# Kernel optimization log

Measured on AMD Instinct MI355X. Metric: run time of the kernel, lower is better.

Reference implementation:

```python
import jax, jax.numpy as jnp
import numpy as np

# Each of the 16 soft binary logic ops is a polynomial c0 + c1*a + c2*b + c3*a*b.
# Rows below are the [c0, c1, c2, c3] coefficients for ops 0..15 (same math as bin_op).
_OP_COEF = np.array([
    [0., 0., 0., 0.],   # 0: zeros
    [0., 0., 0., 1.],   # 1: a*b
    [0., 1., 0., -1.],  # 2: a - a*b
    [0., 1., 0., 0.],   # 3: a
    [0., 0., 1., -1.],  # 4: b - a*b
    [0., 0., 1., 0.],   # 5: b
    [0., 1., 1., -2.],  # 6: a + b - 2ab
    [0., 1., 1., -1.],  # 7: a + b - ab
    [1., -1., -1., 1.], # 8: 1 - (a + b - ab)
    [1., -1., -1., 2.], # 9: 1 - (a + b - 2ab)
    [1., 0., -1., 0.],  # 10: 1 - b
    [1., 0., -1., 1.],  # 11: 1 - b + ab
    [1., -1., 0., 0.],  # 12: 1 - a
    [1., -1., 0., 1.],  # 13: 1 - a + ab
    [1., 0., 0., -1.],  # 14: 1 - a*b
    [1., 0., 0., 0.],   # 15: ones
], dtype=np.float32)

K_CLASSES = 10
TAU = 30.0


def logic_layer(x, w, idx_a, idx_b):
    # x: [B, in_dim], w: [out_dim, 16], idx_a/idx_b: [out_dim]
    probs = jax.nn.softmax(w, axis=-1)                 # [O, 16]
    coef = probs @ jnp.asarray(_OP_COEF)               # [O, 4]
    a = x[:, idx_a]                                    # [B, O]
    b = x[:, idx_b]                                    # [B, O]
    # weighted mixture of 16 ops == polynomial in (1, a, b, a*b)
    return coef[:, 0] + coef[:, 1] * a + coef[:, 2] * b + coef[:, 3] * (a * b)


def group_sum(x, k, tau):
    B = x.shape[0]
    return x.reshape(B, k, x.shape[-1] // k).sum(-1) / tau


def setup_inputs() -> dict:
    key = jax.random.key(0)
    ks = jax.random.split(key, 10)
    B, D0, D1, D2, D3 = 4096, 1024, 8192, 8192, 10240
    return {
        "x": jax.random.uniform(ks[0], (B, D0), dtype=jnp.float32),
        "w1": jax.random.normal(ks[1], (D1, 16), dtype=jnp.float32),
        "w2": jax.random.normal(ks[2], (D2, 16), dtype=jnp.float32),
        "w3": jax.random.normal(ks[3], (D3, 16), dtype=jnp.float32),
        "idx_a1": jax.random.randint(ks[4], (D1,), 0, D0, dtype=jnp.int32),
        "idx_b1": jax.random.randint(ks[5], (D1,), 0, D0, dtype=jnp.int32),
        "idx_a2": jax.random.randint(ks[6], (D2,), 0, D1, dtype=jnp.int32),
        "idx_b2": jax.random.randint(ks[7], (D2,), 0, D1, dtype=jnp.int32),
        "idx_a3": jax.random.randint(ks[8], (D3,), 0, D2, dtype=jnp.int32),
        "idx_b3": jax.random.randint(ks[9], (D3,), 0, D2, dtype=jnp.int32),
    }


def reference(x, w1, w2, w3, idx_a1, idx_b1, idx_a2, idx_b2, idx_a3, idx_b3):
    h = logic_layer(x, w1, idx_a1, idx_b1)
    h = logic_layer(h, w2, idx_a2, idx_b2)
    h = logic_layer(h, w3, idx_a3, idx_b3)
    return group_sum(h, K_CLASSES, TAU)   # [B, 10]
```

## Files before the change

kernel.cpp:

```cpp
#include <hip/hip_runtime.h>
#include <hip/hip_fp16.h>
#include <stdint.h>

#define D0 1024
#define D1 8192
#define D2 8192
#define D3 10240
#define B_ROWS 4096

#define SM_XB     0
#define SM_H2     8192
#define SM_CSUM   (8192 + 65536)
#define SM_BYTES  (8192 + 65536 + 160)

__device__ __forceinline__ float4 softmax_coef(const float* __restrict__ w) {
    const float4* wv = (const float4*)w;
    float4 q0 = wv[0], q1 = wv[1], q2 = wv[2], q3 = wv[3];
    float wa[16] = {q0.x, q0.y, q0.z, q0.w, q1.x, q1.y, q1.z, q1.w,
                    q2.x, q2.y, q2.z, q2.w, q3.x, q3.y, q3.z, q3.w};
    float m = wa[0];
#pragma unroll
    for (int i = 1; i < 16; ++i) m = fmaxf(m, wa[i]);
    float e[16], s = 0.f;
#pragma unroll
    for (int i = 0; i < 16; ++i) { e[i] = __expf(wa[i] - m); s += e[i]; }
    float inv = 1.f / s;
    static constexpr float OPC[16][4] = {
        {0.f, 0.f, 0.f, 0.f}, {0.f, 0.f, 0.f, 1.f}, {0.f, 1.f, 0.f, -1.f}, {0.f, 1.f, 0.f, 0.f},
        {0.f, 0.f, 1.f, -1.f}, {0.f, 0.f, 1.f, 0.f}, {0.f, 1.f, 1.f, -2.f}, {0.f, 1.f, 1.f, -1.f},
        {1.f, -1.f, -1.f, 1.f}, {1.f, -1.f, -1.f, 2.f}, {1.f, 0.f, -1.f, 0.f}, {1.f, 0.f, -1.f, 1.f},
        {1.f, -1.f, 0.f, 0.f}, {1.f, -1.f, 0.f, 1.f}, {1.f, 0.f, 0.f, -1.f}, {1.f, 0.f, 0.f, 0.f}};
    float c0 = 0.f, c1 = 0.f, c2 = 0.f, c3 = 0.f;
#pragma unroll
    for (int i = 0; i < 16; ++i) {
        float p = e[i] * inv;
        c0 += p * OPC[i][0];
        c1 += p * OPC[i][1];
        c2 += p * OPC[i][2];
        c3 += p * OPC[i][3];
    }
    return make_float4(c0, c1, c2, c3);
}

__device__ __forceinline__ uint2 pack_coef(float4 c) {
    uint2 r;
    r.x = __builtin_bit_cast(uint32_t, __floats2half2_rn(c.x, c.y));
    r.y = __builtin_bit_cast(uint32_t, __floats2half2_rn(c.z, c.w));
    return r;
}

__global__ __launch_bounds__(64) void prep_kernel(
    const float* __restrict__ w1, const float* __restrict__ w2,
    const float* __restrict__ w3,
    const int* __restrict__ ia1, const int* __restrict__ ib1,
    const int* __restrict__ ia2, const int* __restrict__ ib2,
    const int* __restrict__ ia3, const int* __restrict__ ib3,
    uint2* __restrict__ bcIdx, uint4* __restrict__ bcCoefAB,
    uint2* __restrict__ bcCoefO, uint32_t* __restrict__ d3Idx,
    uint2* __restrict__ d3Coef) {
    int G = blockIdx.x * 64 + threadIdx.x;
    if (G < D2) {
        int g = G;
        int pa = ia2[g], pb = ib2[g];
        float4 cO = softmax_coef(w2 + (size_t)g * 16);
        float4 cA = softmax_coef(w1 + (size_t)pa * 16);
        float4 cB = softmax_coef(w1 + (size_t)pb * 16);
        uint2 xi;
        xi.x = (uint32_t)(ia1[pa] << 3) | ((uint32_t)(ib1[pa] << 3) << 16);
        xi.y = (uint32_t)(ia1[pb] << 3) | ((uint32_t)(ib1[pb] << 3) << 16);
        bcIdx[g] = xi;
        uint2 a = pack_coef(cA), b = pack_coef(cB);
        bcCoefAB[g] = make_uint4(a.x, a.y, b.x, b.y);
        bcCoefO[g] = pack_coef(cO);
    } else {
        int g = G - D2;
        float4 cO = softmax_coef(w3 + (size_t)g * 16);
        d3Idx[g] = (uint32_t)(ia3[g] << 3) | ((uint32_t)(ib3[g] << 3) << 16);
        d3Coef[g] = pack_coef(cO);
    }
}

__device__ __forceinline__ uint2 gate4(uint2 av, uint2 bv, uint2 cf) {
    __half2 p = __builtin_bit_cast(__half2, cf.x);
    __half2 q = __builtin_bit_cast(__half2, cf.y);
    __half2 c0 = __low2half2(p), c1 = __high2half2(p);
    __half2 c2 = __low2half2(q), c3 = __high2half2(q);
    __half2 a01 = __builtin_bit_cast(__half2, av.x);
    __half2 a23 = __builtin_bit_cast(__half2, av.y);
    __half2 b01 = __builtin_bit_cast(__half2, bv.x);
    __half2 b23 = __builtin_bit_cast(__half2, bv.y);
    __half2 h01 = __hfma2(a01, __hfma2(b01, c3, c1), __hfma2(b01, c2, c0));
    __half2 h23 = __hfma2(a23, __hfma2(b23, c3, c1), __hfma2(b23, c2, c0));
    uint2 r;
    r.x = __builtin_bit_cast(uint32_t, h01);
    r.y = __builtin_bit_cast(uint32_t, h23);
    return r;
}

__global__ __launch_bounds__(1024, 8) void fused_kernel(
    const float* __restrict__ x, const uint2* __restrict__ bcIdx,
    const uint4* __restrict__ bcCoefAB, const uint2* __restrict__ bcCoefO,
    const uint32_t* __restrict__ d3Idx, const uint2* __restrict__ d3Coef,
    float* __restrict__ out) {
    extern __shared__ char sm[];
    uint2* xb = (uint2*)(sm + SM_XB);
    uint2* h2 = (uint2*)(sm + SM_H2);
    float* csum = (float*)(sm + SM_CSUM);

    const int t = threadIdx.x;
    const int rowbase = blockIdx.x << 2;

    {
        const float* xp = x + (size_t)rowbase * D0 + t;
        float v0 = xp[0];
        float v1 = xp[D0];
        float v2 = xp[2 * D0];
        float v3 = xp[3 * D0];
        uint2 v;
        v.x = __builtin_bit_cast(uint32_t, __floats2half2_rn(v0, v1));
        v.y = __builtin_bit_cast(uint32_t, __floats2half2_rn(v2, v3));
        xb[t] = v;
    }
    if (t < 40) csum[t] = 0.f;
    __syncthreads();

    for (int k = 0; k < 8; ++k) {
        int g = t + (k << 10);
        uint2 xi = bcIdx[g];
        uint4 cab = bcCoefAB[g];
        uint2 co = bcCoefO[g];
        uint2 aa = *(const uint2*)(sm + (xi.x & 0xffffu));
        uint2 ab = *(const uint2*)(sm + (xi.x >> 16));
        uint2 ba = *(const uint2*)(sm + (xi.y & 0xffffu));
        uint2 bb = *(const uint2*)(sm + (xi.y >> 16));
        uint2 ha = gate4(aa, ab, make_uint2(cab.x, cab.y));
        uint2 hb = gate4(ba, bb, make_uint2(cab.z, cab.w));
        h2[g] = gate4(ha, hb, co);
    }
    __syncthreads();

    {
        const int wv = t >> 6, lane = t & 63;
        const int gbase = wv * 640;
        const int cA = gbase >> 10;
        const int bnd = (cA + 1) << 10;
        float s0[4] = {0.f, 0.f, 0.f, 0.f};
        float s1[4] = {0.f, 0.f, 0.f, 0.f};
#pragma unroll
        for (int j = 0; j < 10; ++j) {
            int gc = gbase + (j << 6);
            int g = gc + lane;
            uint32_t ip = d3Idx[g];
            uint2 cf = d3Coef[g];
            uint2 av = *(const uint2*)(sm + SM_H2 + (ip & 0xffffu));
            uint2 bv = *(const uint2*)(sm + SM_H2 + (ip >> 16));
            uint2 hv = gate4(av, bv, cf);
            __half2 h01 = __builtin_bit_cast(__half2, hv.x);
            __half2 h23 = __builtin_bit_cast(__half2, hv.y);
            float f0 = __low2float(h01), f1 = __high2float(h01);
            float f2 = __low2float(h23), f3 = __high2float(h23);
            if (gc < bnd) {
                s0[0] += f0; s0[1] += f1; s0[2] += f2; s0[3] += f3;
            } else {
                s1[0] += f0; s1[1] += f1; s1[2] += f2; s1[3] += f3;
            }
        }
#pragma unroll
        for (int m = 1; m < 64; m <<= 1) {
#pragma unroll
            for (int r = 0; r < 4; ++r) {
                s0[r] += __shfl_xor(s0[r], m, 64);
                s1[r] += __shfl_xor(s1[r], m, 64);
            }
        }
        if (lane == 0) {
#pragma unroll
            for (int r = 0; r < 4; ++r) atomicAdd(&csum[cA * 4 + r], s0[r]);
            if (gbase + 640 > bnd) {
#pragma unroll
                for (int r = 0; r < 4; ++r) atomicAdd(&csum[(cA + 1) * 4 + r], s1[r]);
            }
        }
    }
    __syncthreads();

    if (t < 40) {
        int c = t >> 2, r = t & 3;
        out[(size_t)(rowbase + r) * 10 + c] = csum[t] * (1.0f / 30.0f);
    }
}

extern "C" void kernel_launch(void* const* d_in, const int* in_sizes, int n_in,
                              void* d_out, int out_size, void* d_ws, size_t ws_size,
                              hipStream_t stream) {
    const float* x = (const float*)d_in[0];
    const float* w1 = (const float*)d_in[1];
    const float* w2 = (const float*)d_in[2];
    const float* w3 = (const float*)d_in[3];
    const int* ia1 = (const int*)d_in[4];
    const int* ib1 = (const int*)d_in[5];
    const int* ia2 = (const int*)d_in[6];
    const int* ib2 = (const int*)d_in[7];
    const int* ia3 = (const int*)d_in[8];
    const int* ib3 = (const int*)d_in[9];
    float* out = (float*)d_out;

    char* p = (char*)d_ws;
    uint2* bcIdx = (uint2*)p;                 p += (size_t)D2 * 8;
    uint4* bcCoefAB = (uint4*)p;              p += (size_t)D2 * 16;
    uint2* bcCoefO = (uint2*)p;               p += (size_t)D2 * 8;
    uint32_t* d3Idx = (uint32_t*)p;           p += (size_t)D3 * 4;
    uint2* d3Coef = (uint2*)p;

    hipFuncSetAttribute(reinterpret_cast<const void*>(fused_kernel),
                        hipFuncAttributeMaxDynamicSharedMemorySize, SM_BYTES);

    prep_kernel<<<(D2 + D3) / 64, 64, 0, stream>>>(
        w1, w2, w3, ia1, ib1, ia2, ib2, ia3, ib3,
        bcIdx, bcCoefAB, bcCoefO, d3Idx, d3Coef);
    fused_kernel<<<B_ROWS / 4, 1024, SM_BYTES, stream>>>(
        x, bcIdx, bcCoefAB, bcCoefO, d3Idx, d3Coef, out);
}
```

Baseline: 107.1 us.

## Pack per-gate metadata into uint4 records and process two gates per thread

Per-gate indices and fp16 coefficients are repacked into 16-byte records. Layer-1/2 uses two arrays (index plus output coef, and A/B coefs), and layer 3 uses one padded record array. Each thread now handles two adjacent gates per iteration with 128-bit loads and prefetches the next iteration's index record before the x staging. This cuts global load instruction count and exposes more memory-level parallelism. In exchange the layer-3 data grows through padding, register pressure rises, and pairs of outputs are summed in fp16 before the float accumulation.

```diff
diff --git a/kernel.cpp b/kernel.cpp
--- a/kernel.cpp
+++ b/kernel.cpp
@@ -55,9 +55,8 @@
     const int* __restrict__ ia1, const int* __restrict__ ib1,
     const int* __restrict__ ia2, const int* __restrict__ ib2,
     const int* __restrict__ ia3, const int* __restrict__ ib3,
-    uint2* __restrict__ bcIdx, uint4* __restrict__ bcCoefAB,
-    uint2* __restrict__ bcCoefO, uint32_t* __restrict__ d3Idx,
-    uint2* __restrict__ d3Coef) {
+    uint4* __restrict__ bcM1, uint4* __restrict__ bcM2,
+    uint4* __restrict__ d3M) {
     int G = blockIdx.x * 64 + threadIdx.x;
     if (G < D2) {
         int g = G;
@@ -65,18 +64,17 @@
         float4 cO = softmax_coef(w2 + (size_t)g * 16);
         float4 cA = softmax_coef(w1 + (size_t)pa * 16);
         float4 cB = softmax_coef(w1 + (size_t)pb * 16);
-        uint2 xi;
-        xi.x = (uint32_t)(ia1[pa] << 3) | ((uint32_t)(ib1[pa] << 3) << 16);
-        xi.y = (uint32_t)(ia1[pb] << 3) | ((uint32_t)(ib1[pb] << 3) << 16);
-        bcIdx[g] = xi;
-        uint2 a = pack_coef(cA), b = pack_coef(cB);
-        bcCoefAB[g] = make_uint4(a.x, a.y, b.x, b.y);
-        bcCoefO[g] = pack_coef(cO);
+        uint32_t xiA = (uint32_t)(ia1[pa] << 3) | ((uint32_t)(ib1[pa] << 3) << 16);
+        uint32_t xiB = (uint32_t)(ia1[pb] << 3) | ((uint32_t)(ib1[pb] << 3) << 16);
+        uint2 o = pack_coef(cO), a = pack_coef(cA), b = pack_coef(cB);
+        bcM1[g] = make_uint4(xiA, xiB, o.x, o.y);
+        bcM2[g] = make_uint4(a.x, a.y, b.x, b.y);
     } else {
         int g = G - D2;
         float4 cO = softmax_coef(w3 + (size_t)g * 16);
-        d3Idx[g] = (uint32_t)(ia3[g] << 3) | ((uint32_t)(ib3[g] << 3) << 16);
-        d3Coef[g] = pack_coef(cO);
+        uint2 o = pack_coef(cO);
+        uint32_t xi = (uint32_t)(ia3[g] << 3) | ((uint32_t)(ib3[g] << 3) << 16);
+        d3M[g] = make_uint4(xi, o.x, o.y, 0u);
     }
 }
 
@@ -98,17 +96,19 @@
 }
 
 __global__ __launch_bounds__(1024, 8) void fused_kernel(
-    const float* __restrict__ x, const uint2* __restrict__ bcIdx,
-    const uint4* __restrict__ bcCoefAB, const uint2* __restrict__ bcCoefO,
-    const uint32_t* __restrict__ d3Idx, const uint2* __restrict__ d3Coef,
+    const float* __restrict__ x, const uint4* __restrict__ bcM1,
+    const uint4* __restrict__ bcM2, const uint4* __restrict__ d3M,
     float* __restrict__ out) {
     extern __shared__ char sm[];
     uint2* xb = (uint2*)(sm + SM_XB);
-    uint2* h2 = (uint2*)(sm + SM_H2);
     float* csum = (float*)(sm + SM_CSUM);
 
     const int t = threadIdx.x;
     const int rowbase = blockIdx.x << 2;
+    const int tg = t << 1;
+
+    uint4 m1a_n = bcM1[tg];
+    uint4 m1b_n = bcM1[tg + 1];
 
     {
         const float* xp = x + (size_t)rowbase * D0 + t;
@@ -124,18 +124,32 @@
     if (t < 40) csum[t] = 0.f;
     __syncthreads();
 
-    for (int k = 0; k < 8; ++k) {
-        int g = t + (k << 10);
-        uint2 xi = bcIdx[g];
-        uint4 cab = bcCoefAB[g];
-        uint2 co = bcCoefO[g];
-        uint2 aa = *(const uint2*)(sm + (xi.x & 0xffffu));
-        uint2 ab = *(const uint2*)(sm + (xi.x >> 16));
-        uint2 ba = *(const uint2*)(sm + (xi.y & 0xffffu));
-        uint2 bb = *(const uint2*)(sm + (xi.y >> 16));
-        uint2 ha = gate4(aa, ab, make_uint2(cab.x, cab.y));
-        uint2 hb = gate4(ba, bb, make_uint2(cab.z, cab.w));
-        h2[g] = gate4(ha, hb, co);
+#pragma unroll
+    for (int k = 0; k < 4; ++k) {
+        uint4 m1a = m1a_n, m1b = m1b_n;
+        int g = tg + (k << 11);
+        uint4 m2a = bcM2[g];
+        uint4 m2b = bcM2[g + 1];
+        if (k < 3) {
+            int gn = tg + ((k + 1) << 11);
+            m1a_n = bcM1[gn];
+            m1b_n = bcM1[gn + 1];
+        }
+        uint2 aa0 = *(const uint2*)(sm + (m1a.x & 0xffffu));
+        uint2 ab0 = *(const uint2*)(sm + (m1a.x >> 16));
+        uint2 ba0 = *(const uint2*)(sm + (m1a.y & 0xffffu));
+        uint2 bb0 = *(const uint2*)(sm + (m1a.y >> 16));
+        uint2 aa1 = *(const uint2*)(sm + (m1b.x & 0xffffu));
+        uint2 ab1 = *(const uint2*)(sm + (m1b.x >> 16));
+        uint2 ba1 = *(const uint2*)(sm + (m1b.y & 0xffffu));
+        uint2 bb1 = *(const uint2*)(sm + (m1b.y >> 16));
+        uint2 h0 = gate4(gate4(aa0, ab0, make_uint2(m2a.x, m2a.y)),
+                         gate4(ba0, bb0, make_uint2(m2a.z, m2a.w)),
+                         make_uint2(m1a.z, m1a.w));
+        uint2 h1v = gate4(gate4(aa1, ab1, make_uint2(m2b.x, m2b.y)),
+                          gate4(ba1, bb1, make_uint2(m2b.z, m2b.w)),
+                          make_uint2(m1b.z, m1b.w));
+        ((uint4*)(sm + SM_H2))[(k << 10) + t] = make_uint4(h0.x, h0.y, h1v.x, h1v.y);
     }
     __syncthreads();
 
@@ -147,18 +161,23 @@
         float s0[4] = {0.f, 0.f, 0.f, 0.f};
         float s1[4] = {0.f, 0.f, 0.f, 0.f};
 #pragma unroll
-        for (int j = 0; j < 10; ++j) {
-            int gc = gbase + (j << 6);
-            int g = gc + lane;
-            uint32_t ip = d3Idx[g];
-            uint2 cf = d3Coef[g];
-            uint2 av = *(const uint2*)(sm + SM_H2 + (ip & 0xffffu));
-            uint2 bv = *(const uint2*)(sm + SM_H2 + (ip >> 16));
-            uint2 hv = gate4(av, bv, cf);
-            __half2 h01 = __builtin_bit_cast(__half2, hv.x);
-            __half2 h23 = __builtin_bit_cast(__half2, hv.y);
-            float f0 = __low2float(h01), f1 = __high2float(h01);
-            float f2 = __low2float(h23), f3 = __high2float(h23);
+        for (int j = 0; j < 5; ++j) {
+            int gc = gbase + (j << 7);
+            int g = gc + (lane << 1);
+            uint4 ma = d3M[g];
+            uint4 mb = d3M[g + 1];
+            uint2 av0 = *(const uint2*)(sm + SM_H2 + (ma.x & 0xffffu));
+            uint2 bv0 = *(const uint2*)(sm + SM_H2 + (ma.x >> 16));
+            uint2 av1 = *(const uint2*)(sm + SM_H2 + (mb.x & 0xffffu));
+            uint2 bv1 = *(const uint2*)(sm + SM_H2 + (mb.x >> 16));
+            uint2 h0 = gate4(av0, bv0, make_uint2(ma.y, ma.z));
+            uint2 h1v = gate4(av1, bv1, make_uint2(mb.y, mb.z));
+            __half2 p01 = __hadd2(__builtin_bit_cast(__half2, h0.x),
+                                  __builtin_bit_cast(__half2, h1v.x));
+            __half2 p23 = __hadd2(__builtin_bit_cast(__half2, h0.y),
+                                  __builtin_bit_cast(__half2, h1v.y));
+            float f0 = __low2float(p01), f1 = __high2float(p01);
+            float f2 = __low2float(p23), f3 = __high2float(p23);
             if (gc < bnd) {
                 s0[0] += f0; s0[1] += f1; s0[2] += f2; s0[3] += f3;
             } else {
@@ -206,18 +225,14 @@
     float* out = (float*)d_out;
 
     char* p = (char*)d_ws;
-    uint2* bcIdx = (uint2*)p;                 p += (size_t)D2 * 8;
-    uint4* bcCoefAB = (uint4*)p;              p += (size_t)D2 * 16;
-    uint2* bcCoefO = (uint2*)p;               p += (size_t)D2 * 8;
-    uint32_t* d3Idx = (uint32_t*)p;           p += (size_t)D3 * 4;
-    uint2* d3Coef = (uint2*)p;
+    uint4* bcM1 = (uint4*)p;    p += (size_t)D2 * 16;
+    uint4* bcM2 = (uint4*)p;    p += (size_t)D2 * 16;
+    uint4* d3M = (uint4*)p;
 
     hipFuncSetAttribute(reinterpret_cast<const void*>(fused_kernel),
                         hipFuncAttributeMaxDynamicSharedMemorySize, SM_BYTES);
 
     prep_kernel<<<(D2 + D3) / 64, 64, 0, stream>>>(
-        w1, w2, w3, ia1, ib1, ia2, ib2, ia3, ib3,
-        bcIdx, bcCoefAB, bcCoefO, d3Idx, d3Coef);
-    fused_kernel<<<B_ROWS / 4, 1024, SM_BYTES, stream>>>(
-        x, bcIdx, bcCoefAB, bcCoefO, d3Idx, d3Coef, out);
-}
+        w1, w2, w3, ia1, ib1, ia2, ib2, ia3, ib3, bcM1, bcM2, d3M);
+    fused_kernel<<<B_ROWS / 4, 1024, SM_BYTES, stream>>>(x, bcM1, bcM2, d3M, out);
+}
```

Result: no change. 106.9 us (-0.2%).

## Recompute layer-2 gates per layer-3 output to eliminate shared intermediate buffer

Applied to the files above, without the earlier changes.

Flattens the three-layer gate tree so each layer-3 output directly gathers its four layer-1 input pairs from the staged input row, recomputing layer-1 and layer-2 gates instead of storing layer-2 results in shared memory. The prep kernel now precomputes per-output composite index and coefficient tables, and the main kernel uses 512 threads with about 8 KB of LDS and one fewer barrier. This trades roughly double gate arithmetic and more metadata loads for much higher occupancy and less LDS traffic.

```diff
diff --git a/kernel.cpp b/kernel.cpp
--- a/kernel.cpp
+++ b/kernel.cpp
@@ -7,11 +7,6 @@
 #define D2 8192
 #define D3 10240
 #define B_ROWS 4096
-
-#define SM_XB     0
-#define SM_H2     8192
-#define SM_CSUM   (8192 + 65536)
-#define SM_BYTES  (8192 + 65536 + 160)
 
 __device__ __forceinline__ float4 softmax_coef(const float* __restrict__ w) {
     const float4* wv = (const float4*)w;
@@ -49,35 +44,33 @@
     return r;
 }
 
-__global__ __launch_bounds__(64) void prep_kernel(
+__global__ __launch_bounds__(256) void prep_kernel(
     const float* __restrict__ w1, const float* __restrict__ w2,
     const float* __restrict__ w3,
     const int* __restrict__ ia1, const int* __restrict__ ib1,
     const int* __restrict__ ia2, const int* __restrict__ ib2,
     const int* __restrict__ ia3, const int* __restrict__ ib3,
-    uint2* __restrict__ bcIdx, uint4* __restrict__ bcCoefAB,
-    uint2* __restrict__ bcCoefO, uint32_t* __restrict__ d3Idx,
-    uint2* __restrict__ d3Coef) {
-    int G = blockIdx.x * 64 + threadIdx.x;
-    if (G < D2) {
-        int g = G;
-        int pa = ia2[g], pb = ib2[g];
-        float4 cO = softmax_coef(w2 + (size_t)g * 16);
-        float4 cA = softmax_coef(w1 + (size_t)pa * 16);
-        float4 cB = softmax_coef(w1 + (size_t)pb * 16);
-        uint2 xi;
-        xi.x = (uint32_t)(ia1[pa] << 3) | ((uint32_t)(ib1[pa] << 3) << 16);
-        xi.y = (uint32_t)(ia1[pb] << 3) | ((uint32_t)(ib1[pb] << 3) << 16);
-        bcIdx[g] = xi;
-        uint2 a = pack_coef(cA), b = pack_coef(cB);
-        bcCoefAB[g] = make_uint4(a.x, a.y, b.x, b.y);
-        bcCoefO[g] = pack_coef(cO);
-    } else {
-        int g = G - D2;
-        float4 cO = softmax_coef(w3 + (size_t)g * 16);
-        d3Idx[g] = (uint32_t)(ia3[g] << 3) | ((uint32_t)(ib3[g] << 3) << 16);
-        d3Coef[g] = pack_coef(cO);
-    }
+    uint4* __restrict__ M0, uint4* __restrict__ M1, uint4* __restrict__ M2,
+    uint4* __restrict__ M3, uint2* __restrict__ M4) {
+    int g = blockIdx.x * 256 + threadIdx.x;
+    int p0 = ia3[g], p1 = ib3[g];
+    int a0 = ia2[p0], b0 = ib2[p0];
+    int a1 = ia2[p1], b1 = ib2[p1];
+    uint32_t x0 = (uint32_t)(ia1[a0] << 3) | ((uint32_t)(ib1[a0] << 3) << 16);
+    uint32_t x1 = (uint32_t)(ia1[b0] << 3) | ((uint32_t)(ib1[b0] << 3) << 16);
+    uint32_t x2 = (uint32_t)(ia1[a1] << 3) | ((uint32_t)(ib1[a1] << 3) << 16);
+    uint32_t x3 = (uint32_t)(ia1[b1] << 3) | ((uint32_t)(ib1[b1] << 3) << 16);
+    M0[g] = make_uint4(x0, x1, x2, x3);
+    uint2 cA0 = pack_coef(softmax_coef(w1 + (size_t)a0 * 16));
+    uint2 cB0 = pack_coef(softmax_coef(w1 + (size_t)b0 * 16));
+    M1[g] = make_uint4(cA0.x, cA0.y, cB0.x, cB0.y);
+    uint2 cA1 = pack_coef(softmax_coef(w1 + (size_t)a1 * 16));
+    uint2 cB1 = pack_coef(softmax_coef(w1 + (size_t)b1 * 16));
+    M2[g] = make_uint4(cA1.x, cA1.y, cB1.x, cB1.y);
+    uint2 cP0 = pack_coef(softmax_coef(w2 + (size_t)p0 * 16));
+    uint2 cP1 = pack_coef(softmax_coef(w2 + (size_t)p1 * 16));
+    M3[g] = make_uint4(cP0.x, cP0.y, cP1.x, cP1.y);
+    M4[g] = pack_coef(softmax_coef(w3 + (size_t)g * 16));
 }
 
 __device__ __forceinline__ uint2 gate4(uint2 av, uint2 bv, uint2 cf) {
@@ -97,89 +90,87 @@
     return r;
 }
 
-__global__ __launch_bounds__(1024, 8) void fused_kernel(
-    const float* __restrict__ x, const uint2* __restrict__ bcIdx,
-    const uint4* __restrict__ bcCoefAB, const uint2* __restrict__ bcCoefO,
-    const uint32_t* __restrict__ d3Idx, const uint2* __restrict__ d3Coef,
+__global__ __launch_bounds__(512, 8) void fused_kernel(
+    const float* __restrict__ x, const uint4* __restrict__ M0,
+    const uint4* __restrict__ M1, const uint4* __restrict__ M2,
+    const uint4* __restrict__ M3, const uint2* __restrict__ M4,
     float* __restrict__ out) {
-    extern __shared__ char sm[];
-    uint2* xb = (uint2*)(sm + SM_XB);
-    uint2* h2 = (uint2*)(sm + SM_H2);
-    float* csum = (float*)(sm + SM_CSUM);
+    __shared__ char sm[8192 + 160];
+    uint2* xb = (uint2*)sm;
+    float* csum = (float*)(sm + 8192);
 
     const int t = threadIdx.x;
     const int rowbase = blockIdx.x << 2;
+    const int wv = t >> 6, lane = t & 63;
+    const int gbase = wv * 1280;
+
+    uint4 m0_n = M0[gbase + lane];
 
     {
-        const float* xp = x + (size_t)rowbase * D0 + t;
-        float v0 = xp[0];
-        float v1 = xp[D0];
-        float v2 = xp[2 * D0];
-        float v3 = xp[3 * D0];
-        uint2 v;
-        v.x = __builtin_bit_cast(uint32_t, __floats2half2_rn(v0, v1));
-        v.y = __builtin_bit_cast(uint32_t, __floats2half2_rn(v2, v3));
-        xb[t] = v;
+        const float* xp = x + (size_t)rowbase * D0;
+#pragma unroll
+        for (int c = t; c < D0; c += 512) {
+            uint2 v;
+            v.x = __builtin_bit_cast(uint32_t, __floats2half2_rn(xp[c], xp[D0 + c]));
+            v.y = __builtin_bit_cast(uint32_t, __floats2half2_rn(xp[2 * D0 + c], xp[3 * D0 + c]));
+            xb[c] = v;
+        }
     }
     if (t < 40) csum[t] = 0.f;
     __syncthreads();
 
-    for (int k = 0; k < 8; ++k) {
-        int g = t + (k << 10);
-        uint2 xi = bcIdx[g];
-        uint4 cab = bcCoefAB[g];
-        uint2 co = bcCoefO[g];
-        uint2 aa = *(const uint2*)(sm + (xi.x & 0xffffu));
-        uint2 ab = *(const uint2*)(sm + (xi.x >> 16));
-        uint2 ba = *(const uint2*)(sm + (xi.y & 0xffffu));
-        uint2 bb = *(const uint2*)(sm + (xi.y >> 16));
-        uint2 ha = gate4(aa, ab, make_uint2(cab.x, cab.y));
-        uint2 hb = gate4(ba, bb, make_uint2(cab.z, cab.w));
-        h2[g] = gate4(ha, hb, co);
-    }
-    __syncthreads();
-
-    {
-        const int wv = t >> 6, lane = t & 63;
-        const int gbase = wv * 640;
-        const int cA = gbase >> 10;
-        const int bnd = (cA + 1) << 10;
-        float s0[4] = {0.f, 0.f, 0.f, 0.f};
-        float s1[4] = {0.f, 0.f, 0.f, 0.f};
-#pragma unroll
-        for (int j = 0; j < 10; ++j) {
-            int gc = gbase + (j << 6);
-            int g = gc + lane;
-            uint32_t ip = d3Idx[g];
-            uint2 cf = d3Coef[g];
-            uint2 av = *(const uint2*)(sm + SM_H2 + (ip & 0xffffu));
-            uint2 bv = *(const uint2*)(sm + SM_H2 + (ip >> 16));
-            uint2 hv = gate4(av, bv, cf);
-            __half2 h01 = __builtin_bit_cast(__half2, hv.x);
-            __half2 h23 = __builtin_bit_cast(__half2, hv.y);
-            float f0 = __low2float(h01), f1 = __high2float(h01);
-            float f2 = __low2float(h23), f3 = __high2float(h23);
-            if (gc < bnd) {
-                s0[0] += f0; s0[1] += f1; s0[2] += f2; s0[3] += f3;
-            } else {
-                s1[0] += f0; s1[1] += f1; s1[2] += f2; s1[3] += f3;
-            }
-        }
-#pragma unroll
-        for (int m = 1; m < 64; m <<= 1) {
-#pragma unroll
-            for (int r = 0; r < 4; ++r) {
-                s0[r] += __shfl_xor(s0[r], m, 64);
-                s1[r] += __shfl_xor(s1[r], m, 64);
-            }
-        }
-        if (lane == 0) {
-#pragma unroll
-            for (int r = 0; r < 4; ++r) atomicAdd(&csum[cA * 4 + r], s0[r]);
-            if (gbase + 640 > bnd) {
-#pragma unroll
-                for (int r = 0; r < 4; ++r) atomicAdd(&csum[(cA + 1) * 4 + r], s1[r]);
-            }
+    const int cA = gbase >> 10;
+    const int bnd = (cA + 1) << 10;
+    float s0[4] = {0.f, 0.f, 0.f, 0.f};
+    float s1[4] = {0.f, 0.f, 0.f, 0.f};
+#pragma unroll
+    for (int j = 0; j < 20; ++j) {
+        int g = gbase + (j << 6) + lane;
+        uint4 m0 = m0_n;
+        if (j < 19) m0_n = M0[g + 64];
+        uint2 aa = *(const uint2*)(sm + (m0.x & 0xffffu));
+        uint2 ab = *(const uint2*)(sm + (m0.x >> 16));
+        uint2 ba = *(const uint2*)(sm + (m0.y & 0xffffu));
+        uint2 bb = *(const uint2*)(sm + (m0.y >> 16));
+        uint2 ca = *(const uint2*)(sm + (m0.z & 0xffffu));
+        uint2 cb = *(const uint2*)(sm + (m0.z >> 16));
+        uint2 da = *(const uint2*)(sm + (m0.w & 0xffffu));
+        uint2 db = *(const uint2*)(sm + (m0.w >> 16));
+        uint4 m1 = M1[g];
+        uint4 m2 = M2[g];
+        uint4 m3 = M3[g];
+        uint2 m4 = M4[g];
+        uint2 hA0 = gate4(aa, ab, make_uint2(m1.x, m1.y));
+        uint2 hB0 = gate4(ba, bb, make_uint2(m1.z, m1.w));
+        uint2 hA1 = gate4(ca, cb, make_uint2(m2.x, m2.y));
+        uint2 hB1 = gate4(da, db, make_uint2(m2.z, m2.w));
+        uint2 hP0 = gate4(hA0, hB0, make_uint2(m3.x, m3.y));
+        uint2 hP1 = gate4(hA1, hB1, make_uint2(m3.z, m3.w));
+        uint2 h = gate4(hP0, hP1, m4);
+        __half2 h01 = __builtin_bit_cast(__half2, h.x);
+        __half2 h23 = __builtin_bit_cast(__half2, h.y);
+        float f0 = __low2float(h01), f1 = __high2float(h01);
+        float f2 = __low2float(h23), f3 = __high2float(h23);
+        if (gbase + (j << 6) < bnd) {
+            s0[0] += f0; s0[1] += f1; s0[2] += f2; s0[3] += f3;
+        } else {
+            s1[0] += f0; s1[1] += f1; s1[2] += f2; s1[3] += f3;
+        }
+    }
+#pragma unroll
+    for (int m = 1; m < 64; m <<= 1) {
+#pragma unroll
+        for (int r = 0; r < 4; ++r) {
+            s0[r] += __shfl_xor(s0[r], m, 64);
+            s1[r] += __shfl_xor(s1[r], m, 64);
+        }
+    }
+    if (lane == 0) {
+#pragma unroll
+        for (int r = 0; r < 4; ++r) atomicAdd(&csum[cA * 4 + r], s0[r]);
+        if (gbase + 1280 > bnd) {
+#pragma unroll
+            for (int r = 0; r < 4; ++r) atomicAdd(&csum[(cA + 1) * 4 + r], s1[r]);
         }
     }
     __syncthreads();
@@ -206,18 +197,13 @@
     float* out = (float*)d_out;
 
     char* p = (char*)d_ws;
-    uint2* bcIdx = (uint2*)p;                 p += (size_t)D2 * 8;
-    uint4* bcCoefAB = (uint4*)p;              p += (size_t)D2 * 16;
-    uint2* bcCoefO = (uint2*)p;               p += (size_t)D2 * 8;
-    uint32_t* d3Idx = (uint32_t*)p;           p += (size_t)D3 * 4;
-    uint2* d3Coef = (uint2*)p;
-
-    hipFuncSetAttribute(reinterpret_cast<const void*>(fused_kernel),
-                        hipFuncAttributeMaxDynamicSharedMemorySize, SM_BYTES);
-
-    prep_kernel<<<(D2 + D3) / 64, 64, 0, stream>>>(
-        w1, w2, w3, ia1, ib1, ia2, ib2, ia3, ib3,
-        bcIdx, bcCoefAB, bcCoefO, d3Idx, d3Coef);
-    fused_kernel<<<B_ROWS / 4, 1024, SM_BYTES, stream>>>(
-        x, bcIdx, bcCoefAB, bcCoefO, d3Idx, d3Coef, out);
-}
+    uint4* M0 = (uint4*)p;  p += (size_t)D3 * 16;
+    uint4* M1 = (uint4*)p;  p += (size_t)D3 * 16;
+    uint4* M2 = (uint4*)p;  p += (size_t)D3 * 16;
+    uint4* M3 = (uint4*)p;  p += (size_t)D3 * 16;
+    uint2* M4 = (uint2*)p;
+
+    prep_kernel<<<D3 / 256, 256, 0, stream>>>(
+        w1, w2, w3, ia1, ib1, ia2, ib2, ia3, ib3, M0, M1, M2, M3, M4);
+    fused_kernel<<<B_ROWS / 4, 512, 0, stream>>>(x, M0, M1, M2, M3, M4, out);
+}
```

Measured after the change: 116.8 us. 9.0% more time.
